# Kernel optimization log

Hardware: AMD Instinct MI355X
Metric: run time of the kernel (lower is better)

## Reference

```python
import jax, jax.numpy as jnp
from jax import lax
import numpy as np

SEQ, BATCH, IN, H = 512, 256, 180, 8


def _lstm_layer(x, w_ih, w_hh, b_ih, b_hh):
    # x: [S, B, I]; PyTorch gate order: i, f, g, o stacked along 4H
    S, B, _ = x.shape
    Hh = w_hh.shape[1]
    # input contribution for all timesteps at once (one big GEMM)
    xg = jnp.einsum('sbi,gi->sbg', x, w_ih) + b_ih + b_hh  # [S, B, 4H]

    def step(carry, xt):
        h, c = carry
        g = xt + h @ w_hh.T  # [B, 4H]
        i, f, gg, o = jnp.split(g, 4, axis=-1)
        i = jax.nn.sigmoid(i)
        f = jax.nn.sigmoid(f)
        gg = jnp.tanh(gg)
        o = jax.nn.sigmoid(o)
        c = f * c + i * gg
        h = o * jnp.tanh(c)
        return (h, c), h

    init = (jnp.zeros((B, Hh), x.dtype), jnp.zeros((B, Hh), x.dtype))
    _, ys = lax.scan(step, init, xg)
    return ys  # [S, B, H]


def setup_inputs() -> dict:
    key = jax.random.key(0)
    ks = jax.random.split(key, 11)
    s = 1.0 / np.sqrt(H)  # PyTorch LSTM init scale
    return {
        'x': jax.random.normal(ks[0], (SEQ, BATCH, IN), jnp.float32),
        'w_ih0': jax.random.uniform(ks[1], (4 * H, IN), jnp.float32, -s, s),
        'w_hh0': jax.random.uniform(ks[2], (4 * H, H), jnp.float32, -s, s),
        'b_ih0': jax.random.uniform(ks[3], (4 * H,), jnp.float32, -s, s),
        'b_hh0': jax.random.uniform(ks[4], (4 * H,), jnp.float32, -s, s),
        'w_ih1': jax.random.uniform(ks[5], (4 * H, H), jnp.float32, -s, s),
        'w_hh1': jax.random.uniform(ks[6], (4 * H, H), jnp.float32, -s, s),
        'b_ih1': jax.random.uniform(ks[7], (4 * H,), jnp.float32, -s, s),
        'b_hh1': jax.random.uniform(ks[8], (4 * H,), jnp.float32, -s, s),
        'w_reg': jax.random.uniform(ks[9], (2, H), jnp.float32, -s, s),
        'b_reg': jax.random.uniform(ks[10], (2,), jnp.float32, -s, s),
    }


def reference(x, w_ih0, w_hh0, b_ih0, b_hh0, w_ih1, w_hh1, b_ih1, b_hh1, w_reg, b_reg):
    h1 = _lstm_layer(x, w_ih0, w_hh0, b_ih0, b_hh0)   # [S, B, H]
    h2 = _lstm_layer(h1, w_ih1, w_hh1, b_ih1, b_hh1)  # [S, B, H]
    S, B, Hh = h2.shape
    flat = h2.reshape(S * B, Hh)
    return flat @ w_reg.T + b_reg  # [S*B, 2]
```

## Files before the change

### kernel.cpp

```cpp
#include <hip/hip_runtime.h>

#define S_  512
#define B_  256
#define NIN 180

typedef float v2 __attribute__((ext_vector_type(2)));

#define SSIG  -1.4426950408889634f
#define STANH -2.8853900817779268f

#define QP_X1 0xB1
#define QP_X2 0x4E
#define QP_X3 0x1B
#define ROR4  0x124
#define ROR8  0x128

template<int CTRL>
__device__ __forceinline__ float dppf(float x) {
    return __uint_as_float((unsigned)__builtin_amdgcn_update_dpp(
        0, (int)__float_as_uint(x), CTRL, 0xF, 0xF, true));
}

#define ROTS8(h, r) do { \
    r[0] = (h); \
    r[1] = dppf<QP_X1>(h); \
    r[2] = dppf<QP_X2>(h); \
    r[3] = dppf<QP_X3>(h); \
    r[4] = dppf<ROR4>(h); \
    r[5] = dppf<QP_X1>(r[4]); \
    r[6] = dppf<QP_X2>(r[4]); \
    r[7] = dppf<QP_X3>(r[4]); \
} while (0)

__global__ __launch_bounds__(256) void xg_gemm(
    const float* __restrict__ x, const float* __restrict__ w,
    const float* __restrict__ bi, const float* __restrict__ bh,
    float* __restrict__ xg2)
{
    __shared__ float wt[NIN][32];
    __shared__ float bias[32];
    const int tid = threadIdx.x;
    for (int idx = tid; idx < NIN * 32; idx += 256) {
        int c = idx / NIN, i = idx - c * NIN;
        int t = c >> 2, e = c & 3;
        int g = (t >> 2) * 8 + (t & 3) * 2 + (e >> 1) + ((e & 1) << 4);
        float sc = ((g >> 3) == 2) ? STANH : SSIG;
        wt[i][c] = sc * w[g * NIN + i];
    }
    if (tid < 32) {
        int c = tid, t = c >> 2, e = c & 3;
        int g = (t >> 2) * 8 + (t & 3) * 2 + (e >> 1) + ((e & 1) << 4);
        float sc = ((g >> 3) == 2) ? STANH : SSIG;
        bias[c] = sc * (bi[g] + bh[g]);
    }
    __syncthreads();

    const int rg = tid >> 3;
    const int t8 = tid & 7;
    const int s  = blockIdx.x;
    const int b0 = rg * 8;
    const float* xr = x + ((size_t)s * B_ + b0) * NIN;

    v2 acc[8][2];
    #pragma unroll
    for (int r = 0; r < 8; ++r) { acc[r][0] = v2{0.f, 0.f}; acc[r][1] = v2{0.f, 0.f}; }

    float4 xb[3][8];
    #pragma unroll
    for (int d = 0; d < 3; ++d)
        #pragma unroll
        for (int r = 0; r < 8; ++r)
            xb[d][r] = *(const float4*)(xr + (size_t)r * NIN + 4 * d);

    auto GSTEP = [&](int ii, int d, bool pref) {
        float4 xn[8];
        if (pref) {
            #pragma unroll
            for (int r = 0; r < 8; ++r)
                xn[r] = *(const float4*)(xr + (size_t)r * NIN + 4 * (ii + 3));
        }
        #pragma unroll
        for (int e = 0; e < 4; ++e) {
            float4 wv = *(const float4*)&wt[4 * ii + e][t8 * 4];
            v2 wlo = v2{wv.x, wv.y}, whi = v2{wv.z, wv.w};
            #pragma unroll
            for (int r = 0; r < 8; ++r) {
                float xe = (e == 0) ? xb[d][r].x : (e == 1) ? xb[d][r].y
                         : (e == 2) ? xb[d][r].z : xb[d][r].w;
                v2 xv = v2{xe, xe};
                acc[r][0] = __builtin_elementwise_fma(wlo, xv, acc[r][0]);
                acc[r][1] = __builtin_elementwise_fma(whi, xv, acc[r][1]);
            }
        }
        if (pref) {
            #pragma unroll
            for (int r = 0; r < 8; ++r) xb[d][r] = xn[r];
        }
    };

    for (int r = 0; r < 14; ++r) {
        GSTEP(3 * r + 0, 0, true);
        GSTEP(3 * r + 1, 1, true);
        GSTEP(3 * r + 2, 2, true);
    }
    GSTEP(42, 0, false);
    GSTEP(43, 1, false);
    GSTEP(44, 2, false);

    float4 bv = *(const float4*)&bias[t8 * 4];
    const int toff = (t8 >> 2) * 16 + (t8 & 3) * 4;
    #pragma unroll
    for (int r = 0; r < 8; ++r) {
        int b = b0 + r;
        float4 o;
        o.x = acc[r][0].x + bv.x;
        o.y = acc[r][0].y + bv.y;
        o.z = acc[r][1].x + bv.z;
        o.w = acc[r][1].y + bv.w;
        size_t base = ((size_t)s * 64 + (b >> 2)) * 128 + (b & 3) * 32 + toff;
        *(float4*)(xg2 + base) = o;
    }
}

__global__ __launch_bounds__(128, 1) void lstm_scan(
    const float* __restrict__ xg,
    const float* __restrict__ w_hh0,
    const float* __restrict__ w_ih1, const float* __restrict__ w_hh1,
    const float* __restrict__ b_ih1, const float* __restrict__ b_hh1,
    const float* __restrict__ w_reg, const float* __restrict__ b_reg,
    float* __restrict__ out)
{
    __shared__ float abuf[16][128];

    const int lt = threadIdx.x & 63;
    const int j  = lt & 7;
    const int b3 = (lt >> 3) & 1;
    const int cc = lt >> 4;
    const bool b3z = (b3 == 0);
    const int bid = blockIdx.x;

    const int gA = b3 * 8 + j;
    const int gB = (2 + b3) * 8 + j;
    const float sB_ = b3z ? STANH : SSIG;
    const float aB  = b3z ? 2.0f : 1.0f;
    const float bB  = b3z ? -1.0f : 0.0f;

    auto COMBINE2 = [&](float tA, float tB, float& c, float& h) {
        float m  = tA * tB;
        float mr = dppf<ROR8>(m);
        float fa = dppf<ROR8>(tA);
        float ob = dppf<ROR8>(tB);
        float ig = b3z ? m  : mr;
        float f  = b3z ? fa : tA;
        float o  = b3z ? ob : tB;
        c = __builtin_fmaf(f, c, ig);
        float th = __builtin_fmaf(2.0f, __builtin_amdgcn_rcpf(
            1.0f + __builtin_amdgcn_exp2f(STANH * c)), -1.0f);
        h = o * th;
    };

    if (threadIdx.x < 64) {
        v2 w0p[8], wi1p[8];
        #pragma unroll
        for (int m = 0; m < 8; ++m) {
            int k = j ^ m;
            w0p[m]  = v2{SSIG * w_hh0[gA * 8 + k], sB_ * w_hh0[gB * 8 + k]};
            wi1p[m] = v2{SSIG * w_ih1[gA * 8 + k], sB_ * w_ih1[gB * 8 + k]};
        }
        const v2 b1p = v2{SSIG * (b_ih1[gA] + b_hh1[gA]),
                          sB_  * (b_ih1[gB] + b_hh1[gB])};

        float h0p = 0.f, c0v = 0.f;
        const float* xrow = xg + (size_t)bid * 128;
        v2 xq[8];
        #pragma unroll
        for (int k2 = 0; k2 < 8; ++k2) {
            xq[k2] = *(const v2*)(xrow + lt * 2);
            xrow += 8192;
        }

        auto ASTEP = [&](v2& xr, int slot, bool store, bool pref) {
            v2 xc = xr;
            if (pref) { xr = *(const v2*)(xrow + lt * 2); xrow += 8192; }
            float r0[8];
            ROTS8(h0p, r0);
            v2 a0 = xc, a1p = b1p;
            #pragma unroll
            for (int m = 0; m < 8; ++m) {
                v2 rm = v2{r0[m], r0[m]};
                a0  = __builtin_elementwise_fma(w0p[m], rm, a0);
                a1p = __builtin_elementwise_fma(wi1p[m], rm, a1p);
            }
            if (store) *(v2*)&abuf[slot][lt * 2] = a1p;
            float eA = __builtin_amdgcn_exp2f(a0.x);
            float eB = __builtin_amdgcn_exp2f(a0.y);
            float tA = __builtin_amdgcn_rcpf(1.0f + eA);
            float tB = __builtin_fmaf(aB, __builtin_amdgcn_rcpf(1.0f + eB), bB);
            COMBINE2(tA, tB, c0v, h0p);
        };

        ASTEP(xq[0], 0, false, true);
        ASTEP(xq[1], 0, true, true);
        ASTEP(xq[2], 1, true, true);
        ASTEP(xq[3], 2, true, true);
        __syncthreads();
        ASTEP(xq[4], 3, true, true);
        ASTEP(xq[5], 4, true, true);
        ASTEP(xq[6], 5, true, true);
        ASTEP(xq[7], 6, true, true);
        __syncthreads();
        for (int m = 0; m < 31; ++m) {
            #pragma unroll
            for (int k = 0; k < 16; ++k) {
                ASTEP(xq[k & 7], (7 + k) & 15, true, true);
                if ((k & 3) == 3) __syncthreads();
            }
        }
        #pragma unroll
        for (int k = 0; k < 8; ++k) {
            ASTEP(xq[k], (7 + k) & 15, true, false);
            if ((k & 3) == 3) __syncthreads();
        }
        {
            float r0[8];
            ROTS8(h0p, r0);
            v2 a1p = b1p;
            #pragma unroll
            for (int m = 0; m < 8; ++m) {
                v2 rm = v2{r0[m], r0[m]};
                a1p = __builtin_elementwise_fma(wi1p[m], rm, a1p);
            }
            *(v2*)&abuf[15][lt * 2] = a1p;
            __syncthreads();
        }
    } else {
        v2 wh1p[8];
        float wrl[8];
        #pragma unroll
        for (int m = 0; m < 8; ++m) {
            int k = j ^ m;
            wh1p[m] = v2{SSIG * w_hh1[gA * 8 + k], sB_ * w_hh1[gB * 8 + k]};
            wrl[m]  = w_reg[b3 * 8 + k];
        }
        const float br  = b_reg[b3];
        const bool isl  = (j == 0);
        float* op = out + (size_t)(bid * 4 + cc) * 2 + b3;

        float h1p = 0.f, c1v = 0.f;

        auto BSTEP = [&](int slot, bool doproj) {
            v2 a1 = *(const v2*)&abuf[slot][lt * 2];
            float r1[8];
            ROTS8(h1p, r1);
            #pragma unroll
            for (int m = 0; m < 8; ++m) {
                v2 rm = v2{r1[m], r1[m]};
                a1 = __builtin_elementwise_fma(wh1p[m], rm, a1);
            }
            float eA = __builtin_amdgcn_exp2f(a1.x);
            float eB = __builtin_amdgcn_exp2f(a1.y);
            float tA = __builtin_amdgcn_rcpf(1.0f + eA);
            float tB = __builtin_fmaf(aB, __builtin_amdgcn_rcpf(1.0f + eB), bB);
            if (doproj) {
                float p = br;
                #pragma unroll
                for (int m = 0; m < 8; ++m) p = __builtin_fmaf(wrl[m], r1[m], p);
                if (isl) *op = p;
                op += 512;
            }
            COMBINE2(tA, tB, c1v, h1p);
        };

        __syncthreads();
        __syncthreads();
        #pragma unroll
        for (int k = 0; k < 16; ++k) {
            BSTEP(k, k != 0);
            if ((k & 3) == 3) __syncthreads();
        }
        for (int m = 1; m < 31; ++m) {
            #pragma unroll
            for (int k = 0; k < 16; ++k) {
                BSTEP(k, true);
                if ((k & 3) == 3) __syncthreads();
            }
        }
        #pragma unroll
        for (int k = 0; k < 8; ++k) {
            BSTEP(k, true);
            if ((k & 3) == 3) __syncthreads();
        }
        __syncthreads();
        #pragma unroll
        for (int k = 8; k < 16; ++k) BSTEP(k, true);
        {
            float r1[8];
            ROTS8(h1p, r1);
            float p = br;
            #pragma unroll
            for (int m = 0; m < 8; ++m) p = __builtin_fmaf(wrl[m], r1[m], p);
            if (isl) *op = p;
        }
    }
}

extern "C" void kernel_launch(void* const* d_in, const int* in_sizes, int n_in,
                              void* d_out, int out_size, void* d_ws, size_t ws_size,
                              hipStream_t stream) {
    (void)in_sizes; (void)n_in; (void)out_size; (void)ws_size;
    const float* x     = (const float*)d_in[0];
    const float* w_ih0 = (const float*)d_in[1];
    const float* w_hh0 = (const float*)d_in[2];
    const float* b_ih0 = (const float*)d_in[3];
    const float* b_hh0 = (const float*)d_in[4];
    const float* w_ih1 = (const float*)d_in[5];
    const float* w_hh1 = (const float*)d_in[6];
    const float* b_ih1 = (const float*)d_in[7];
    const float* b_hh1 = (const float*)d_in[8];
    const float* w_reg = (const float*)d_in[9];
    const float* b_reg = (const float*)d_in[10];
    float* out = (float*)d_out;
    float* xg2 = (float*)d_ws;

    xg_gemm<<<512, 256, 0, stream>>>(x, w_ih0, b_ih0, b_hh0, xg2);
    lstm_scan<<<64, 128, 0, stream>>>(xg2, w_hh0, w_ih1, w_hh1, b_ih1, b_hh1,
                                      w_reg, b_reg, out);
}
```

Baseline: 129.6 us.

## Split LSTM scan into three-wave pipeline and move projection to separate kernel

Scan kernel now uses three wavefronts: wave 0 runs the layer-0 recurrence and writes h0 into a shared ring, wave 1 computes the layer-1 input projection from that ring, and wave 2 runs the layer-1 recurrence. This takes the w_ih1 matvec off both recurrent critical paths. The FMA chains are split into two partial sums to shorten dependency latency, and the regression projection moves to a separate proj_k kernel when workspace allows, with h stored to global memory. The input GEMM uses twice as many blocks with half the rows each, adding an extra launch and a global h round-trip.

```diff
diff --git a/kernel.cpp b/kernel.cpp
--- a/kernel.cpp
+++ b/kernel.cpp
@@ -57,26 +57,26 @@
 
     const int rg = tid >> 3;
     const int t8 = tid & 7;
-    const int s  = blockIdx.x;
-    const int b0 = rg * 8;
+    const int s  = blockIdx.x >> 1;
+    const int b0 = (blockIdx.x & 1) * 128 + rg * 4;
     const float* xr = x + ((size_t)s * B_ + b0) * NIN;
 
-    v2 acc[8][2];
+    v2 acc[4][2];
     #pragma unroll
-    for (int r = 0; r < 8; ++r) { acc[r][0] = v2{0.f, 0.f}; acc[r][1] = v2{0.f, 0.f}; }
-
-    float4 xb[3][8];
+    for (int r = 0; r < 4; ++r) { acc[r][0] = v2{0.f,0.f}; acc[r][1] = v2{0.f,0.f}; }
+
+    float4 xb[3][4];
     #pragma unroll
     for (int d = 0; d < 3; ++d)
         #pragma unroll
-        for (int r = 0; r < 8; ++r)
+        for (int r = 0; r < 4; ++r)
             xb[d][r] = *(const float4*)(xr + (size_t)r * NIN + 4 * d);
 
     auto GSTEP = [&](int ii, int d, bool pref) {
-        float4 xn[8];
+        float4 xn[4];
         if (pref) {
             #pragma unroll
-            for (int r = 0; r < 8; ++r)
+            for (int r = 0; r < 4; ++r)
                 xn[r] = *(const float4*)(xr + (size_t)r * NIN + 4 * (ii + 3));
         }
         #pragma unroll
@@ -84,7 +84,7 @@
             float4 wv = *(const float4*)&wt[4 * ii + e][t8 * 4];
             v2 wlo = v2{wv.x, wv.y}, whi = v2{wv.z, wv.w};
             #pragma unroll
-            for (int r = 0; r < 8; ++r) {
+            for (int r = 0; r < 4; ++r) {
                 float xe = (e == 0) ? xb[d][r].x : (e == 1) ? xb[d][r].y
                          : (e == 2) ? xb[d][r].z : xb[d][r].w;
                 v2 xv = v2{xe, xe};
@@ -94,7 +94,7 @@
         }
         if (pref) {
             #pragma unroll
-            for (int r = 0; r < 8; ++r) xb[d][r] = xn[r];
+            for (int r = 0; r < 4; ++r) xb[d][r] = xn[r];
         }
     };
 
@@ -110,7 +110,7 @@
     float4 bv = *(const float4*)&bias[t8 * 4];
     const int toff = (t8 >> 2) * 16 + (t8 & 3) * 4;
     #pragma unroll
-    for (int r = 0; r < 8; ++r) {
+    for (int r = 0; r < 4; ++r) {
         int b = b0 + r;
         float4 o;
         o.x = acc[r][0].x + bv.x;
@@ -122,20 +122,24 @@
     }
 }
 
-__global__ __launch_bounds__(128, 1) void lstm_scan(
+template<bool HB>
+__global__ __launch_bounds__(192, 1) void lstm_scan(
     const float* __restrict__ xg,
     const float* __restrict__ w_hh0,
     const float* __restrict__ w_ih1, const float* __restrict__ w_hh1,
     const float* __restrict__ b_ih1, const float* __restrict__ b_hh1,
     const float* __restrict__ w_reg, const float* __restrict__ b_reg,
-    float* __restrict__ out)
+    float* __restrict__ hb, float* __restrict__ out)
 {
-    __shared__ float abuf[16][128];
-
-    const int lt = threadIdx.x & 63;
-    const int j  = lt & 7;
-    const int b3 = (lt >> 3) & 1;
-    const int cc = lt >> 4;
+    __shared__ float ring0[16][64];
+    __shared__ float ring1[16][128];
+
+    const int tid = threadIdx.x;
+    const int wid = tid >> 6;
+    const int lt  = tid & 63;
+    const int j   = lt & 7;
+    const int b3  = (lt >> 3) & 1;
+    const int cc  = lt >> 4;
     const bool b3z = (b3 == 0);
     const int bid = blockIdx.x;
 
@@ -159,78 +163,73 @@
         h = o * th;
     };
 
-    if (threadIdx.x < 64) {
-        v2 w0p[8], wi1p[8];
+    if (wid == 0) {
+        v2 w0p[8];
         #pragma unroll
         for (int m = 0; m < 8; ++m) {
             int k = j ^ m;
-            w0p[m]  = v2{SSIG * w_hh0[gA * 8 + k], sB_ * w_hh0[gB * 8 + k]};
+            w0p[m] = v2{SSIG * w_hh0[gA * 8 + k], sB_ * w_hh0[gB * 8 + k]};
+        }
+        float h0p = 0.f, c0v = 0.f;
+
+        const float* xbase = xg + (size_t)bid * 128 + lt * 2;
+        v2 xq[8];
+        #pragma unroll
+        for (int k = 0; k < 8; ++k) xq[k] = *(const v2*)(xbase + (size_t)k * 8192);
+
+        for (int hh = 0; hh < 64; ++hh) {
+            const float* pre = xbase + (size_t)((8 * hh + 8) & 511) * 8192;
+            const int sb8 = (hh & 1) * 8;
+            #pragma unroll
+            for (int k = 0; k < 8; ++k) {
+                v2 xc = xq[k];
+                xq[k] = *(const v2*)(pre + (size_t)k * 8192);
+                float r0[8];
+                ROTS8(h0p, r0);
+                v2 a0L = __builtin_elementwise_fma(w0p[0], v2{r0[0], r0[0]}, xc);
+                v2 a0H = w0p[4] * v2{r0[4], r0[4]};
+                #pragma unroll
+                for (int m = 1; m < 4; ++m) {
+                    a0L = __builtin_elementwise_fma(w0p[m], v2{r0[m], r0[m]}, a0L);
+                    a0H = __builtin_elementwise_fma(w0p[m + 4], v2{r0[m + 4], r0[m + 4]}, a0H);
+                }
+                v2 a0 = a0L + a0H;
+                float eA = __builtin_amdgcn_exp2f(a0.x);
+                float eB = __builtin_amdgcn_exp2f(a0.y);
+                float tA = __builtin_amdgcn_rcpf(1.0f + eA);
+                float tB = __builtin_fmaf(aB, __builtin_amdgcn_rcpf(1.0f + eB), bB);
+                COMBINE2(tA, tB, c0v, h0p);
+                ring0[sb8 + k][lt] = h0p;
+                if (k == 3 || k == 7) __syncthreads();
+            }
+        }
+        __syncthreads();
+    } else if (wid == 1) {
+        v2 wi1p[8];
+        #pragma unroll
+        for (int m = 0; m < 8; ++m) {
+            int k = j ^ m;
             wi1p[m] = v2{SSIG * w_ih1[gA * 8 + k], sB_ * w_ih1[gB * 8 + k]};
         }
         const v2 b1p = v2{SSIG * (b_ih1[gA] + b_hh1[gA]),
                           sB_  * (b_ih1[gB] + b_hh1[gB])};
 
-        float h0p = 0.f, c0v = 0.f;
-        const float* xrow = xg + (size_t)bid * 128;
-        v2 xq[8];
-        #pragma unroll
-        for (int k2 = 0; k2 < 8; ++k2) {
-            xq[k2] = *(const v2*)(xrow + lt * 2);
-            xrow += 8192;
-        }
-
-        auto ASTEP = [&](v2& xr, int slot, bool store, bool pref) {
-            v2 xc = xr;
-            if (pref) { xr = *(const v2*)(xrow + lt * 2); xrow += 8192; }
-            float r0[8];
-            ROTS8(h0p, r0);
-            v2 a0 = xc, a1p = b1p;
-            #pragma unroll
-            for (int m = 0; m < 8; ++m) {
-                v2 rm = v2{r0[m], r0[m]};
-                a0  = __builtin_elementwise_fma(w0p[m], rm, a0);
-                a1p = __builtin_elementwise_fma(wi1p[m], rm, a1p);
+        __syncthreads();
+        for (int p = 1; p <= 128; ++p) {
+            const int sb = ((p - 1) & 3) * 4;
+            float h0v[4];
+            #pragma unroll
+            for (int k = 0; k < 4; ++k) h0v[k] = ring0[sb + k][lt];
+            #pragma unroll
+            for (int k = 0; k < 4; ++k) {
+                float r0[8];
+                ROTS8(h0v[k], r0);
+                v2 a = __builtin_elementwise_fma(wi1p[0], v2{r0[0], r0[0]}, b1p);
+                #pragma unroll
+                for (int m = 1; m < 8; ++m)
+                    a = __builtin_elementwise_fma(wi1p[m], v2{r0[m], r0[m]}, a);
+                *(v2*)&ring1[sb + k][lt * 2] = a;
             }
-            if (store) *(v2*)&abuf[slot][lt * 2] = a1p;
-            float eA = __builtin_amdgcn_exp2f(a0.x);
-            float eB = __builtin_amdgcn_exp2f(a0.y);
-            float tA = __builtin_amdgcn_rcpf(1.0f + eA);
-            float tB = __builtin_fmaf(aB, __builtin_amdgcn_rcpf(1.0f + eB), bB);
-            COMBINE2(tA, tB, c0v, h0p);
-        };
-
-        ASTEP(xq[0], 0, false, true);
-        ASTEP(xq[1], 0, true, true);
-        ASTEP(xq[2], 1, true, true);
-        ASTEP(xq[3], 2, true, true);
-        __syncthreads();
-        ASTEP(xq[4], 3, true, true);
-        ASTEP(xq[5], 4, true, true);
-        ASTEP(xq[6], 5, true, true);
-        ASTEP(xq[7], 6, true, true);
-        __syncthreads();
-        for (int m = 0; m < 31; ++m) {
-            #pragma unroll
-            for (int k = 0; k < 16; ++k) {
-                ASTEP(xq[k & 7], (7 + k) & 15, true, true);
-                if ((k & 3) == 3) __syncthreads();
-            }
-        }
-        #pragma unroll
-        for (int k = 0; k < 8; ++k) {
-            ASTEP(xq[k], (7 + k) & 15, true, false);
-            if ((k & 3) == 3) __syncthreads();
-        }
-        {
-            float r0[8];
-            ROTS8(h0p, r0);
-            v2 a1p = b1p;
-            #pragma unroll
-            for (int m = 0; m < 8; ++m) {
-                v2 rm = v2{r0[m], r0[m]};
-                a1p = __builtin_elementwise_fma(wi1p[m], rm, a1p);
-            }
-            *(v2*)&abuf[15][lt * 2] = a1p;
             __syncthreads();
         }
     } else {
@@ -244,70 +243,87 @@
         }
         const float br  = b_reg[b3];
         const bool isl  = (j == 0);
-        float* op = out + (size_t)(bid * 4 + cc) * 2 + b3;
-
+        float* hrow = hb + (size_t)(bid * 4 + cc) * 8 + j;
+        float* op   = out + (size_t)(bid * 4 + cc) * 2 + b3;
         float h1p = 0.f, c1v = 0.f;
 
-        auto BSTEP = [&](int slot, bool doproj) {
-            v2 a1 = *(const v2*)&abuf[slot][lt * 2];
+        auto BODY4 = [&](int p, bool last) {
+            const int sb = ((p - 2) & 3) * 4;
+            v2 a1in[4];
+            #pragma unroll
+            for (int k = 0; k < 4; ++k) a1in[k] = *(const v2*)&ring1[sb + k][lt * 2];
+            #pragma unroll
+            for (int k = 0; k < 4; ++k) {
+                float r1[8];
+                ROTS8(h1p, r1);
+                v2 aL = __builtin_elementwise_fma(wh1p[0], v2{r1[0], r1[0]}, a1in[k]);
+                v2 aH = wh1p[4] * v2{r1[4], r1[4]};
+                #pragma unroll
+                for (int m = 1; m < 4; ++m) {
+                    aL = __builtin_elementwise_fma(wh1p[m], v2{r1[m], r1[m]}, aL);
+                    aH = __builtin_elementwise_fma(wh1p[m + 4], v2{r1[m + 4], r1[m + 4]}, aH);
+                }
+                v2 a1 = aL + aH;
+                float eA = __builtin_amdgcn_exp2f(a1.x);
+                float eB = __builtin_amdgcn_exp2f(a1.y);
+                float tA = __builtin_amdgcn_rcpf(1.0f + eA);
+                float tB = __builtin_fmaf(aB, __builtin_amdgcn_rcpf(1.0f + eB), bB);
+                if (!HB) {
+                    if (p > 2 || k > 0) {
+                        float pp = br;
+                        #pragma unroll
+                        for (int m = 0; m < 8; ++m) pp = __builtin_fmaf(wrl[m], r1[m], pp);
+                        if (isl) *op = pp;
+                        op += 512;
+                    }
+                }
+                COMBINE2(tA, tB, c1v, h1p);
+                if (HB) {
+                    if (b3z) *hrow = h1p;
+                    hrow += 2048;
+                }
+            }
+            if (!last) __syncthreads();
+        };
+
+        __syncthreads();
+        __syncthreads();
+        for (int p = 2; p <= 128; ++p) BODY4(p, false);
+        BODY4(129, true);
+        if (!HB) {
             float r1[8];
             ROTS8(h1p, r1);
-            #pragma unroll
-            for (int m = 0; m < 8; ++m) {
-                v2 rm = v2{r1[m], r1[m]};
-                a1 = __builtin_elementwise_fma(wh1p[m], rm, a1);
-            }
-            float eA = __builtin_amdgcn_exp2f(a1.x);
-            float eB = __builtin_amdgcn_exp2f(a1.y);
-            float tA = __builtin_amdgcn_rcpf(1.0f + eA);
-            float tB = __builtin_fmaf(aB, __builtin_amdgcn_rcpf(1.0f + eB), bB);
-            if (doproj) {
-                float p = br;
-                #pragma unroll
-                for (int m = 0; m < 8; ++m) p = __builtin_fmaf(wrl[m], r1[m], p);
-                if (isl) *op = p;
-                op += 512;
-            }
-            COMBINE2(tA, tB, c1v, h1p);
-        };
-
-        __syncthreads();
-        __syncthreads();
-        #pragma unroll
-        for (int k = 0; k < 16; ++k) {
-            BSTEP(k, k != 0);
-            if ((k & 3) == 3) __syncthreads();
-        }
-        for (int m = 1; m < 31; ++m) {
-            #pragma unroll
-            for (int k = 0; k < 16; ++k) {
-                BSTEP(k, true);
-                if ((k & 3) == 3) __syncthreads();
-            }
-        }
-        #pragma unroll
-        for (int k = 0; k < 8; ++k) {
-            BSTEP(k, true);
-            if ((k & 3) == 3) __syncthreads();
-        }
-        __syncthreads();
-        #pragma unroll
-        for (int k = 8; k < 16; ++k) BSTEP(k, true);
-        {
-            float r1[8];
-            ROTS8(h1p, r1);
-            float p = br;
-            #pragma unroll
-            for (int m = 0; m < 8; ++m) p = __builtin_fmaf(wrl[m], r1[m], p);
-            if (isl) *op = p;
-        }
-    }
+            float pp = br;
+            #pragma unroll
+            for (int m = 0; m < 8; ++m) pp = __builtin_fmaf(wrl[m], r1[m], pp);
+            if (isl) *op = pp;
+        }
+    }
+}
+
+__global__ __launch_bounds__(256) void proj_k(
+    const float* __restrict__ hbuf, const float* __restrict__ w_reg,
+    const float* __restrict__ b_reg, float* __restrict__ out)
+{
+    const int s = blockIdx.x, t = threadIdx.x;
+    const float* hr = hbuf + ((size_t)s * B_ + t) * 8;
+    float4 h0 = *(const float4*)hr;
+    float4 h1 = *(const float4*)(hr + 4);
+    float hv[8] = {h0.x, h0.y, h0.z, h0.w, h1.x, h1.y, h1.z, h1.w};
+    float p0 = b_reg[0], p1 = b_reg[1];
+    #pragma unroll
+    for (int m = 0; m < 8; ++m) {
+        p0 = __builtin_fmaf(w_reg[m], hv[m], p0);
+        p1 = __builtin_fmaf(w_reg[8 + m], hv[m], p1);
+    }
+    float2 o = {p0, p1};
+    *(float2*)(out + ((size_t)s * B_ + t) * 2) = o;
 }
 
 extern "C" void kernel_launch(void* const* d_in, const int* in_sizes, int n_in,
                               void* d_out, int out_size, void* d_ws, size_t ws_size,
                               hipStream_t stream) {
-    (void)in_sizes; (void)n_in; (void)out_size; (void)ws_size;
+    (void)in_sizes; (void)n_in; (void)out_size;
     const float* x     = (const float*)d_in[0];
     const float* w_ih0 = (const float*)d_in[1];
     const float* w_hh0 = (const float*)d_in[2];
@@ -321,8 +337,19 @@
     const float* b_reg = (const float*)d_in[10];
     float* out = (float*)d_out;
     float* xg2 = (float*)d_ws;
-
-    xg_gemm<<<512, 256, 0, stream>>>(x, w_ih0, b_ih0, b_hh0, xg2);
-    lstm_scan<<<64, 128, 0, stream>>>(xg2, w_hh0, w_ih1, w_hh1, b_ih1, b_hh1,
-                                      w_reg, b_reg, out);
-}
+    const size_t XG_BYTES = (size_t)S_ * 64 * 128 * 4;
+    const size_t HB_BYTES = (size_t)S_ * B_ * 8 * 4;
+    float* hbuf = (float*)((char*)d_ws + XG_BYTES);
+
+    xg_gemm<<<1024, 256, 0, stream>>>(x, w_ih0, b_ih0, b_hh0, xg2);
+    if (ws_size >= XG_BYTES + HB_BYTES) {
+        lstm_scan<true><<<64, 192, 0, stream>>>(xg2, w_hh0, w_ih1, w_hh1,
+                                                b_ih1, b_hh1, w_reg, b_reg,
+                                                hbuf, out);
+        proj_k<<<512, 256, 0, stream>>>(hbuf, w_reg, b_reg, out);
+    } else {
+        lstm_scan<false><<<64, 192, 0, stream>>>(xg2, w_hh0, w_ih1, w_hh1,
+                                                 b_ih1, b_hh1, w_reg, b_reg,
+                                                 xg2, out);
+    }
+}
```

Result: faster. 111.8 us (-13.7%).
